# Performance work log

Measured on AMD Instinct MI355X. Metric: run time of the kernel, lower is better.

## Reference

```python
import jax, jax.numpy as jnp
import numpy as np

N = 50000
E = 640000
IN_DIM = 23
HID = 128
NUM_CLASS = 12


def setup_inputs() -> dict:
    key = jax.random.key(0)
    ks = jax.random.split(key, 12)
    x = jax.random.normal(ks[0], (N, IN_DIM), dtype=jnp.float32)
    edge_index = jax.random.randint(ks[1], (2, E), 0, N, dtype=jnp.int32)

    def glorot(k, shape):
        fan_in, fan_out = shape
        lim = np.sqrt(6.0 / (fan_in + fan_out)).astype(np.float32)
        return jax.random.uniform(k, shape, jnp.float32, -lim, lim)

    W1 = glorot(ks[2], (IN_DIM, HID)); b1 = jnp.zeros((HID,), jnp.float32)
    W2 = glorot(ks[3], (HID, HID));    b2 = jnp.zeros((HID,), jnp.float32)
    W3 = glorot(ks[4], (HID, HID));    b3 = jnp.zeros((HID,), jnp.float32)
    Wc1 = glorot(ks[5], (HID, 64));    bc1 = jnp.zeros((64,), jnp.float32)
    Wc2 = glorot(ks[6], (64, NUM_CLASS)); bc2 = jnp.zeros((NUM_CLASS,), jnp.float32)
    return {"x": x, "edge_index": edge_index,
            "W1": W1, "b1": b1, "W2": W2, "b2": b2, "W3": W3, "b3": b3,
            "Wc1": Wc1, "bc1": bc1, "Wc2": Wc2, "bc2": bc2}


def _gcn_norm(edge_index, n_nodes):
    # add self loops, compute symmetric normalization D^-1/2 (A+I) D^-1/2
    loop = jnp.arange(n_nodes, dtype=edge_index.dtype)
    src = jnp.concatenate([edge_index[0], loop])
    dst = jnp.concatenate([edge_index[1], loop])
    deg = jax.ops.segment_sum(jnp.ones_like(dst, dtype=jnp.float32), dst,
                              num_segments=n_nodes)
    dinv = jax.lax.rsqrt(deg)  # deg >= 1 due to self loops
    norm = dinv[src] * dinv[dst]  # [E + N]
    return src, dst, norm


def _gcn_layer(h, W, b, src, dst, norm, n_nodes):
    h = h @ W                          # linear (bias applied after aggregation, per PyG)
    msg = h[src] * norm[:, None]       # gather + scale
    out = jax.ops.segment_sum(msg, dst, num_segments=n_nodes)  # scatter-add
    return out + b


def reference(x, edge_index, W1, b1, W2, b2, W3, b3, Wc1, bc1, Wc2, bc2):
    n = x.shape[0]
    src, dst, norm = _gcn_norm(edge_index, n)
    h = jnp.tanh(_gcn_layer(x, W1, b1, src, dst, norm, n))
    h = jnp.tanh(_gcn_layer(h, W2, b2, src, dst, norm, n))
    h = jnp.tanh(_gcn_layer(h, W3, b3, src, dst, norm, n))
    # dropout is identity in eval mode
    out = h @ Wc1 + bc1
    out = out @ Wc2 + bc2
    return out
```

## Files before the change

### kernel.cpp

```cpp
#include <hip/hip_runtime.h>
#include <math.h>

#define NN 50000
#define EE 640000
#define IND 23
#define HID 128
#define MIDD 64
#define NCLS 12
#define NB 49
#define QS 32766.0f
#define INVQS (1.0f / 32766.0f)
#define BSH 7
#define NBK 391
#define CHUNK 4096
#define NPB 157
#define PADB 6250
#define GB16 3125

typedef short short8v __attribute__((ext_vector_type(8)));
typedef short short4v __attribute__((ext_vector_type(4)));
typedef float f32x4 __attribute__((ext_vector_type(4)));
typedef unsigned long long u64;

__device__ __forceinline__ short f2bf(float f) {
    unsigned u = __float_as_uint(f);
    unsigned r = (u + 0x7FFFu + ((u >> 16) & 1u)) >> 16;
    return (short)r;
}
__device__ __forceinline__ float bf2f(short s) {
    return __uint_as_float(((unsigned)(unsigned short)s) << 16);
}
__device__ __forceinline__ float fast_tanh(float x) {
    float t = __expf(-2.f * fabsf(x));
    float r = (1.f - t) / (1.f + t);
    return copysignf(r, x);
}

__global__ __launch_bounds__(256) void k_pre(const int* __restrict__ dst,
                                             int* __restrict__ cnt,
                                             const float* __restrict__ Wc1,
                                             const float* __restrict__ bc1,
                                             const float* __restrict__ Wc2,
                                             const float* __restrict__ bc2,
                                             float* __restrict__ Wcc,
                                             float* __restrict__ bcc,
                                             const float* __restrict__ W2,
                                             const float* __restrict__ W3,
                                             short* __restrict__ w2hi,
                                             short* __restrict__ w2lo,
                                             short* __restrict__ w3hi,
                                             short* __restrict__ w3lo,
                                             const float* __restrict__ W1,
                                             short* __restrict__ w1hi,
                                             short* __restrict__ w1lo) {
    const int bid = blockIdx.x;
    const int tid = threadIdx.x;
    if (bid < 2500) {
        int i = bid * 256 + tid;
        if (i < EE) atomicAdd(&cnt[dst[i]], 1);
        return;
    }
    if (bid < 2506) {
        int t = (bid - 2500) * 256 + tid;
        if (t < HID * NCLS) {
            int k = t / NCLS, c = t % NCLS;
            float s = 0.f;
#pragma unroll 8
            for (int j = 0; j < MIDD; ++j) s += Wc1[k * MIDD + j] * Wc2[j * NCLS + c];
            Wcc[t] = s;
        }
        if (t < NCLS) {
            float s = bc2[t];
#pragma unroll 8
            for (int j = 0; j < MIDD; ++j) s += bc1[j] * Wc2[j * NCLS + t];
            bcc[t] = s;
        }
        return;
    }
    if (bid < 2634) {
        int bb = bid - 2506;
        const float* W = (bb < 64) ? W2 : W3;
        short* hi = (bb < 64) ? w2hi : w3hi;
        short* lo = (bb < 64) ? w2lo : w3lo;
        int i = (bb & 63) * 256 + tid;
        int k = i >> 7, c = i & 127;
        float w = W[i];
        short h = f2bf(w);
        short l = f2bf(w - bf2f(h));
        hi[((k >> 3) * 128 + c) * 8 + (k & 7)] = h;
        lo[((k >> 3) * 128 + c) * 8 + (k & 7)] = l;
        return;
    }
    int i = (bid - 2634) * 256 + tid;
    int k = i >> 7, c = i & 127;
    float w = (k < IND) ? W1[k * HID + c] : 0.f;
    short h = f2bf(w);
    short l = f2bf(w - bf2f(h));
    w1hi[((k >> 3) * 128 + c) * 8 + (k & 7)] = h;
    w1lo[((k >> 3) * 128 + c) * 8 + (k & 7)] = l;
}

__global__ __launch_bounds__(256) void k_scan_local(const int* __restrict__ cnt,
                                                    int* __restrict__ row_ptr,
                                                    float* __restrict__ dinv,
                                                    int* __restrict__ sums) {
    __shared__ int wtot[4];
    const int tid = threadIdx.x;
    const int wid = tid >> 6, lane = tid & 63;
    const int base = blockIdx.x * 1024 + tid * 4;
    int v[4];
#pragma unroll
    for (int t = 0; t < 4; ++t) {
        int i = base + t;
        v[t] = (i < NN) ? cnt[i] : 0;
        if (i < NN) dinv[i] = rsqrtf((float)v[t] + 1.0f);
    }
    int slocal = v[0] + v[1] + v[2] + v[3];
    int val = slocal;
#pragma unroll
    for (int off = 1; off < 64; off <<= 1) {
        int t = __shfl_up(val, off, 64);
        if (lane >= off) val += t;
    }
    if (lane == 63) wtot[wid] = val;
    __syncthreads();
    int woff = 0;
#pragma unroll
    for (int w = 0; w < 4; ++w) woff += (w < wid) ? wtot[w] : 0;
    int run = woff + val - slocal;
#pragma unroll
    for (int t = 0; t < 4; ++t) {
        int i = base + t;
        if (i < NN) row_ptr[i] = run;
        run += v[t];
    }
    if (tid == 255) sums[blockIdx.x] = woff + val;
}

__global__ __launch_bounds__(256) void k_scan_apply2(int* __restrict__ row_ptr,
                                                     const int* __restrict__ sums,
                                                     int* __restrict__ bcurA) {
    __shared__ int so;
    const int tid = threadIdx.x;
    if (tid < 64) {
        int a = (tid < (int)blockIdx.x) ? sums[tid] : 0;
        int b = (tid < NB) ? sums[tid] : 0;
#pragma unroll
        for (int off = 32; off; off >>= 1) {
            a += __shfl_down(a, off, 64);
            b += __shfl_down(b, off, 64);
        }
        if (tid == 0) {
            so = a;
            if (blockIdx.x == NB - 1) row_ptr[NN] = b;
        }
    }
    __syncthreads();
    const int o = so;
    const int base = blockIdx.x * 1024 + tid * 4;
#pragma unroll
    for (int t = 0; t < 4; ++t) {
        int i = base + t;
        if (i < NN) {
            int rp = row_ptr[i] + o;
            row_ptr[i] = rp;
            if ((i & 127) == 0) bcurA[i >> BSH] = rp;
        }
    }
}

__global__ __launch_bounds__(256) void k_part(const int* __restrict__ src,
                                              const int* __restrict__ dst,
                                              const float* __restrict__ dinv,
                                              int* __restrict__ bcurA,
                                              u64* __restrict__ sw_g,
                                              int* __restrict__ d_g,
                                              const float* __restrict__ x,
                                              float* __restrict__ xp) {
    const int bid = blockIdx.x;
    const int tid = threadIdx.x;
    if (bid >= NPB) {
        int i = (bid - NPB) * 256 + tid;
        int node = i >> 5, f = i & 31;
        xp[i] = (f < IND) ? x[node * IND + f] * dinv[node] : 0.f;
        return;
    }
    __shared__ int hist[NBK], base[NBK], cur[NBK], gb[NBK];
    __shared__ u64 lsw[CHUNK];
    __shared__ int ld[CHUNK];
    const int e0 = bid * CHUNK;
    const int total = min(CHUNK, EE - e0);
    for (int t = tid; t < NBK; t += 256) hist[t] = 0;
    __syncthreads();
    int sv[16], dv[16];
#pragma unroll
    for (int t = 0; t < 16; ++t) {
        int i = e0 + t * 256 + tid;
        if (i < EE) {
            sv[t] = src[i];
            dv[t] = dst[i];
            atomicAdd(&hist[dv[t] >> BSH], 1);
        } else dv[t] = -1;
    }
    __syncthreads();
    if (tid < 64) {
        int carry = 0;
        for (int c = 0; c < NBK; c += 64) {
            int idx = c + tid;
            int v = (idx < NBK) ? hist[idx] : 0;
            int sc = v;
#pragma unroll
            for (int off = 1; off < 64; off <<= 1) {
                int tv = __shfl_up(sc, off, 64);
                if (tid >= off) sc += tv;
            }
            if (idx < NBK) base[idx] = carry + sc - v;
            carry += __shfl(sc, 63, 64);
        }
    }
    __syncthreads();
    for (int t = tid; t < NBK; t += 256) {
        cur[t] = base[t];
        gb[t] = hist[t] ? atomicAdd(&bcurA[t], hist[t]) : 0;
    }
    __syncthreads();
#pragma unroll
    for (int t = 0; t < 16; ++t) {
        if (dv[t] >= 0) {
            int b = dv[t] >> BSH;
            int r = atomicAdd(&cur[b], 1);
            lsw[r] = (unsigned)sv[t] |
                     ((u64)__float_as_uint(dinv[sv[t]]) << 32);
            ld[r] = dv[t];
        }
    }
    __syncthreads();
    for (int j = tid; j < total; j += 256) {
        int d = ld[j];
        int b = d >> BSH;
        int gpos = gb[b] + (j - base[b]);
        sw_g[gpos] = lsw[j];
        d_g[gpos] = d;
    }
}

__global__ __launch_bounds__(256) void k_sort(const int* __restrict__ row_ptr,
                                              const u64* __restrict__ sw_g,
                                              const int* __restrict__ d_g,
                                              u64* __restrict__ e_sn) {
    __shared__ int rloc[129];
    __shared__ int curl[128];
    __shared__ u64 osw[3072];
    const int bid = blockIdx.x, tid = threadIdx.x;
    const int n0 = bid << BSH;
    const int nlast = min(128, NN - n0);
    if (tid <= nlast) rloc[tid] = row_ptr[n0 + tid];
    if (tid < 128) curl[tid] = 0;
    __syncthreads();
    const int rbeg = rloc[0];
    const int cnt = rloc[nlast] - rbeg;
    for (int j = tid; j < cnt; j += 256) {
        int d = d_g[rbeg + j];
        int li = d - n0;
        int r = atomicAdd(&curl[li], 1);
        int pl = (rloc[li] - rbeg) + r;
        u64 v = sw_g[rbeg + j];
        if (pl < 3072) osw[pl] = v;
        else e_sn[rbeg + pl] = v;
    }
    __syncthreads();
    const int lim = min(cnt, 3072);
    for (int j = tid; j < lim; j += 256) e_sn[rbeg + j] = osw[j];
}

__global__ __launch_bounds__(256) void k_aggx(const float* __restrict__ xp,
                                              const int* __restrict__ row_ptr,
                                              const int2* __restrict__ e_sn,
                                              const float* __restrict__ dinv,
                                              short4v* __restrict__ axh,
                                              short4v* __restrict__ axl) {
    const int tid = threadIdx.x;
    const int i = blockIdx.x * 4 + (tid >> 6);
    const int lane = tid & 63;
    const int slot = lane >> 3;
    const int f = lane & 7;
    const float4* xp4 = (const float4*)xp;
    const int beg = row_ptr[i];
    const int deg = row_ptr[i + 1] - beg;
    float4 acc = make_float4(0.f, 0.f, 0.f, 0.f);
    for (int base = 0; base < deg; base += 64) {
        const int cnt = min(64, deg - base);
        int s_l = 0;
        if (lane < cnt) s_l = e_sn[beg + base + lane].x;
        int e = 0;
        for (; e + 8 <= cnt; e += 8) {
            int s = __shfl(s_l, e + slot, 64);
            float4 v = xp4[s * 8 + f];
            acc.x += v.x; acc.y += v.y; acc.z += v.z; acc.w += v.w;
        }
        if (e < cnt) {
            int s = __shfl(s_l, e + slot, 64);
            if (e + slot < cnt) {
                float4 v = xp4[s * 8 + f];
                acc.x += v.x; acc.y += v.y; acc.z += v.z; acc.w += v.w;
            }
        }
    }
#pragma unroll
    for (int off = 32; off >= 8; off >>= 1) {
        acc.x += __shfl_down(acc.x, off, 64);
        acc.y += __shfl_down(acc.y, off, 64);
        acc.z += __shfl_down(acc.z, off, 64);
        acc.w += __shfl_down(acc.w, off, 64);
    }
    if (lane < 8) {
        const float di = dinv[i];
        float4 v = xp4[i * 8 + lane];
        float a[4];
        a[0] = (acc.x + v.x) * di; a[1] = (acc.y + v.y) * di;
        a[2] = (acc.z + v.z) * di; a[3] = (acc.w + v.w) * di;
        short4v h4, l4;
#pragma unroll
        for (int j = 0; j < 4; ++j) {
            short h = f2bf(a[j]);
            h4[j] = h;
            l4[j] = f2bf(a[j] - bf2f(h));
        }
        axh[(size_t)i * 8 + lane] = h4;
        axl[(size_t)i * 8 + lane] = l4;
    }
}

__global__ __launch_bounds__(256) void k_gemm_l1(const short8v* __restrict__ axh8,
                                                 const short8v* __restrict__ axl8,
                                                 const short8v* __restrict__ w1hi8,
                                                 const short8v* __restrict__ w1lo8,
                                                 const float* __restrict__ bias,
                                                 short* __restrict__ qout) {
    const int tid = threadIdx.x;
    const int lane = tid & 63, wv = tid >> 6;
    const int g = lane >> 4, c16 = lane & 15;
    const int rb = blockIdx.x * 16;
    const int colb = wv * 32;
    short8v Ah = axh8[(size_t)(rb + c16) * 4 + g];
    short8v Al = axl8[(size_t)(rb + c16) * 4 + g];
    short8v Bh[2], Bl[2];
#pragma unroll
    for (int ct = 0; ct < 2; ++ct) {
        int wi = g * 128 + colb + ct * 16 + c16;
        Bh[ct] = w1hi8[wi];
        Bl[ct] = w1lo8[wi];
    }
    __builtin_amdgcn_sched_barrier(0);
    f32x4 acc[2];
    acc[0] = f32x4{0.f, 0.f, 0.f, 0.f};
    acc[1] = f32x4{0.f, 0.f, 0.f, 0.f};
#pragma unroll
    for (int ct = 0; ct < 2; ++ct) {
        acc[ct] = __builtin_amdgcn_mfma_f32_16x16x32_bf16(Ah, Bh[ct], acc[ct], 0, 0, 0);
        acc[ct] = __builtin_amdgcn_mfma_f32_16x16x32_bf16(Ah, Bl[ct], acc[ct], 0, 0, 0);
        acc[ct] = __builtin_amdgcn_mfma_f32_16x16x32_bf16(Al, Bh[ct], acc[ct], 0, 0, 0);
    }
#pragma unroll
    for (int ct = 0; ct < 2; ++ct) {
        const int col = colb + ct * 16 + c16;
        const float bb = bias[col];
#pragma unroll
        for (int r = 0; r < 4; ++r) {
            int nd = rb + 4 * g + r;
            float v = fast_tanh(acc[ct][r] + bb);
            qout[nd * HID + col] = (short)__float2int_rn(v * QS);
        }
    }
}

__global__ __launch_bounds__(256) void k_aggq(const short* __restrict__ hq,
                                              const int* __restrict__ row_ptr,
                                              const int2* __restrict__ e_sn,
                                              const float* __restrict__ dinv,
                                              short8v* __restrict__ ah,
                                              short8v* __restrict__ al) {
    const int tid = threadIdx.x;
    const int i = blockIdx.x * 4 + (tid >> 6);
    const int lane = tid & 63;
    const int slot = lane >> 4;
    const int f = lane & 15;
    const short8v* h8 = (const short8v*)hq;
    const int beg = row_ptr[i];
    const int deg = row_ptr[i + 1] - beg;
    float facc[8];
#pragma unroll
    for (int t = 0; t < 8; ++t) facc[t] = 0.f;
    for (int base = 0; base < deg; base += 64) {
        const int cnt = min(64, deg - base);
        int s_l = 0; float n_l = 0.f;
        if (lane < cnt) {
            int2 sn = e_sn[beg + base + lane];
            s_l = sn.x;
            n_l = __int_as_float(sn.y);
        }
        int e = 0;
#pragma unroll 4
        for (; e + 4 <= cnt; e += 4) {
            int s = __shfl(s_l, e + slot, 64);
            float nr = __shfl(n_l, e + slot, 64);
            short8v v = h8[(size_t)s * 16 + f];
#pragma unroll
            for (int t = 0; t < 8; ++t) facc[t] += (float)v[t] * nr;
        }
        if (e < cnt) {
            int s = __shfl(s_l, e + slot, 64);
            float nr = __shfl(n_l, e + slot, 64);
            if (e + slot < cnt) {
                short8v v = h8[(size_t)s * 16 + f];
#pragma unroll
                for (int t = 0; t < 8; ++t) facc[t] += (float)v[t] * nr;
            }
        }
    }
#pragma unroll
    for (int off = 32; off >= 16; off >>= 1)
#pragma unroll
        for (int t = 0; t < 8; ++t) facc[t] += __shfl_down(facc[t], off, 64);
    if (lane < 16) {
        const float di = dinv[i];
        const float sc = di * INVQS;
        short8v v = h8[(size_t)i * 16 + lane];
        short8v hi8, lo8;
#pragma unroll
        for (int t = 0; t < 8; ++t) {
            float o = (facc[t] + di * (float)v[t]) * sc;
            short h = f2bf(o);
            hi8[t] = h;
            lo8[t] = f2bf(o - bf2f(h));
        }
        ah[(size_t)i * 16 + lane] = hi8;
        al[(size_t)i * 16 + lane] = lo8;
    }
}

#define GEMM_CORE16                                                            \
    const int tid = threadIdx.x;                                               \
    const int lane = tid & 63, wv = tid >> 6;                                  \
    const int g = lane >> 4, c16 = lane & 15;                                  \
    const int rb = blockIdx.x * 16;                                            \
    const int colb = wv * 32;                                                  \
    const size_t arow = (size_t)(rb + c16) * 16;                               \
    short8v Ah[4], Al[4], Bh[4][2], Bl[4][2];                                  \
    _Pragma("unroll")                                                          \
    for (int t = 0; t < 4; ++t) {                                              \
        Ah[t] = ah[arow + t * 4 + g];                                          \
        Al[t] = al[arow + t * 4 + g];                                          \
        _Pragma("unroll")                                                      \
        for (int ct = 0; ct < 2; ++ct) {                                       \
            int wi = (t * 4 + g) * 128 + colb + ct * 16 + c16;                 \
            Bh[t][ct] = whi8[wi];                                              \
            Bl[t][ct] = wlo8[wi];                                              \
        }                                                                      \
    }                                                                          \
    __builtin_amdgcn_sched_barrier(0);                                         \
    f32x4 acc[2];                                                              \
    acc[0] = f32x4{0.f, 0.f, 0.f, 0.f};                                        \
    acc[1] = f32x4{0.f, 0.f, 0.f, 0.f};                                        \
    _Pragma("unroll")                                                          \
    for (int t = 0; t < 4; ++t) {                                              \
        _Pragma("unroll")                                                      \
        for (int ct = 0; ct < 2; ++ct) {                                       \
            acc[ct] = __builtin_amdgcn_mfma_f32_16x16x32_bf16(Ah[t], Bh[t][ct], acc[ct], 0, 0, 0); \
            acc[ct] = __builtin_amdgcn_mfma_f32_16x16x32_bf16(Ah[t], Bl[t][ct], acc[ct], 0, 0, 0); \
            acc[ct] = __builtin_amdgcn_mfma_f32_16x16x32_bf16(Al[t], Bh[t][ct], acc[ct], 0, 0, 0); \
        }                                                                      \
    }

__global__ __launch_bounds__(256) void k_gemm_q(const short8v* __restrict__ ah,
                                                const short8v* __restrict__ al,
                                                const short8v* __restrict__ whi8,
                                                const short8v* __restrict__ wlo8,
                                                const float* __restrict__ bias,
                                                short* __restrict__ qout) {
    GEMM_CORE16
#pragma unroll
    for (int ct = 0; ct < 2; ++ct) {
        const int col = colb + ct * 16 + c16;
        const float bb = bias[col];
#pragma unroll
        for (int r = 0; r < 4; ++r) {
            int nd = rb + 4 * g + r;
            float v = fast_tanh(acc[ct][r] + bb);
            qout[nd * HID + col] = (short)__float2int_rn(v * QS);
        }
    }
}

__global__ __launch_bounds__(256) void k_gemm_head(const short8v* __restrict__ ah,
                                                   const short8v* __restrict__ al,
                                                   const short8v* __restrict__ whi8,
                                                   const short8v* __restrict__ wlo8,
                                                   const float* __restrict__ bias,
                                                   const float* __restrict__ Wcc,
                                                   const float* __restrict__ bcc,
                                                   float* __restrict__ outp) {
    __shared__ float WccS[HID * NCLS];
    __shared__ float bccS[NCLS];
    __shared__ float psum[4][16][NCLS];
    {
        const int t0 = threadIdx.x;
        for (int t = t0; t < HID * NCLS; t += 256) WccS[t] = Wcc[t];
        if (t0 < NCLS) bccS[t0] = bcc[t0];
    }
    __syncthreads();
    GEMM_CORE16
    float part[4][NCLS];
#pragma unroll
    for (int r = 0; r < 4; ++r)
#pragma unroll
        for (int c = 0; c < NCLS; ++c) part[r][c] = 0.f;
#pragma unroll
    for (int ct = 0; ct < 2; ++ct) {
        const int col = colb + ct * 16 + c16;
        const float bb = bias[col];
        const float4* wr = (const float4*)&WccS[col * NCLS];
        float4 wa = wr[0], wb2 = wr[1], wc = wr[2];
#pragma unroll
        for (int r = 0; r < 4; ++r) {
            float v = fast_tanh(acc[ct][r] + bb);
            part[r][0]  += v * wa.x;  part[r][1]  += v * wa.y;
            part[r][2]  += v * wa.z;  part[r][3]  += v * wa.w;
            part[r][4]  += v * wb2.x; part[r][5]  += v * wb2.y;
            part[r][6]  += v * wb2.z; part[r][7]  += v * wb2.w;
            part[r][8]  += v * wc.x;  part[r][9]  += v * wc.y;
            part[r][10] += v * wc.z;  part[r][11] += v * wc.w;
        }
    }
#pragma unroll
    for (int off = 8; off; off >>= 1)
#pragma unroll
        for (int r = 0; r < 4; ++r)
#pragma unroll
            for (int c = 0; c < NCLS; ++c)
                part[r][c] += __shfl_down(part[r][c], off, 64);
    if (c16 == 0) {
#pragma unroll
        for (int r = 0; r < 4; ++r)
#pragma unroll
            for (int c = 0; c < NCLS; ++c)
                psum[wv][4 * g + r][c] = part[r][c];
    }
    __syncthreads();
    if (tid < 16 * NCLS) {
        int row = tid / NCLS, c = tid % NCLS;
        float s = bccS[c] + psum[0][row][c] + psum[1][row][c]
                + psum[2][row][c] + psum[3][row][c];
        outp[(rb + row) * NCLS + c] = s;
    }
}


extern "C" void kernel_launch(void* const* d_in, const int* in_sizes, int n_in,
                              void* d_out, int out_size, void* d_ws, size_t ws_size,
                              hipStream_t stream) {
    const float* x    = (const float*)d_in[0];
    const int*   edge = (const int*)d_in[1];
    const int*   src  = edge;
    const int*   dst  = edge + EE;
    const float* W1  = (const float*)d_in[2];  const float* b1  = (const float*)d_in[3];
    const float* W2  = (const float*)d_in[4];  const float* b2  = (const float*)d_in[5];
    const float* W3  = (const float*)d_in[6];  const float* b3  = (const float*)d_in[7];
    const float* Wc1 = (const float*)d_in[8];  const float* bc1 = (const float*)d_in[9];
    const float* Wc2 = (const float*)d_in[10]; const float* bc2 = (const float*)d_in[11];
    float* outp = (float*)d_out;

    char* p = (char*)d_ws;
    int*   cnt     = (int*)p;   p += 200064;
    int*   row_ptr = (int*)p;   p += 200064;
    float* dinv    = (float*)p; p += 200064;
    int*   sums    = (int*)p;   p += 256;
    int*   bcurA   = (int*)p;   p += 2048;
    int2*  e_sn    = (int2*)p;  p += (size_t)EE * 8;
    u64*   sw_g    = (u64*)p;   p += (size_t)EE * 8;
    int*   d_g     = (int*)p;   p += (size_t)EE * 4;
    float* xp      = (float*)p; p += (size_t)NN * 32 * 4;
    short* q       = (short*)p; p += (size_t)NN * HID * 2;
    short8v* ah    = (short8v*)p; p += (size_t)(NN + 16) * 256;
    short8v* al    = (short8v*)p; p += (size_t)(NN + 16) * 256;
    short4v* axh   = (short4v*)p; p += (size_t)(NN + 16) * 64;
    short4v* axl   = (short4v*)p; p += (size_t)(NN + 16) * 64;
    float* Wcc     = (float*)p; p += HID * NCLS * 4;
    float* bcc     = (float*)p; p += 256;
    short* w2hi    = (short*)p; p += 32768;
    short* w2lo    = (short*)p; p += 32768;
    short* w3hi    = (short*)p; p += 32768;
    short* w3lo    = (short*)p; p += 32768;
    short* w1hi    = (short*)p; p += 8192;
    short* w1lo    = (short*)p; p += 8192;

    hipMemsetAsync(cnt, 0, (size_t)NN * 4, stream);
    k_pre        <<<2650, 256, 0, stream>>>(dst, cnt, Wc1, bc1, Wc2, bc2, Wcc, bcc,
                                            W2, W3, w2hi, w2lo, w3hi, w3lo,
                                            W1, w1hi, w1lo);
    k_scan_local <<<NB, 256, 0, stream>>>(cnt, row_ptr, dinv, sums);
    k_scan_apply2<<<NB, 256, 0, stream>>>(row_ptr, sums, bcurA);
    k_part       <<<NPB + PADB, 256, 0, stream>>>(src, dst, dinv, bcurA,
                                                  sw_g, d_g, x, xp);
    k_sort       <<<NBK, 256, 0, stream>>>(row_ptr, sw_g, d_g, (u64*)e_sn);

    k_aggx    <<<NN / 4, 256, 0, stream>>>(xp, row_ptr, e_sn, dinv, axh, axl);
    k_gemm_l1 <<<GB16, 256, 0, stream>>>((const short8v*)axh, (const short8v*)axl,
                                         (const short8v*)w1hi, (const short8v*)w1lo,
                                         b1, q);
    k_aggq     <<<NN / 4, 256, 0, stream>>>(q, row_ptr, e_sn, dinv, ah, al);
    k_gemm_q   <<<GB16, 256, 0, stream>>>(ah, al, (const short8v*)w2hi,
                                          (const short8v*)w2lo, b2, q);
    k_aggq     <<<NN / 4, 256, 0, stream>>>(q, row_ptr, e_sn, dinv, ah, al);
    k_gemm_head<<<GB16, 256, 0, stream>>>(ah, al, (const short8v*)w3hi,
                                          (const short8v*)w3lo, b3, Wcc, bcc, outp);
}
```

Measured before the change: 288.4 us.

## Merge two-pass scan into single-block kernel and widen aggq per-lane loads

Replaces the two-kernel prefix scan (local scan plus apply) with one 1024-thread single-block kernel that walks the node counts in 13 chunks with a running total. This removes a kernel launch at the cost of running the scan serially on one CU. Separately, the aggregation kernel now gives each lane 16 features (two short8 loads) across 8 edge slots instead of 8 features across 4 slots. This doubles the number of edges in flight per wavefront but also doubles per-lane accumulator registers.

```diff
diff --git a/kernel.cpp b/kernel.cpp
--- a/kernel.cpp
+++ b/kernel.cpp
@@ -7,7 +7,6 @@
 #define HID 128
 #define MIDD 64
 #define NCLS 12
-#define NB 49
 #define QS 32766.0f
 #define INVQS (1.0f / 32766.0f)
 #define BSH 7
@@ -100,73 +99,53 @@
     w1lo[((k >> 3) * 128 + c) * 8 + (k & 7)] = l;
 }
 
-__global__ __launch_bounds__(256) void k_scan_local(const int* __restrict__ cnt,
-                                                    int* __restrict__ row_ptr,
-                                                    float* __restrict__ dinv,
-                                                    int* __restrict__ sums) {
-    __shared__ int wtot[4];
+__global__ __launch_bounds__(1024) void k_scan(const int* __restrict__ cnt,
+                                               int* __restrict__ row_ptr,
+                                               float* __restrict__ dinv,
+                                               int* __restrict__ bcurA) {
+    __shared__ int wsum[16];
     const int tid = threadIdx.x;
     const int wid = tid >> 6, lane = tid & 63;
-    const int base = blockIdx.x * 1024 + tid * 4;
-    int v[4];
-#pragma unroll
-    for (int t = 0; t < 4; ++t) {
-        int i = base + t;
-        v[t] = (i < NN) ? cnt[i] : 0;
-        if (i < NN) dinv[i] = rsqrtf((float)v[t] + 1.0f);
-    }
-    int slocal = v[0] + v[1] + v[2] + v[3];
-    int val = slocal;
-#pragma unroll
-    for (int off = 1; off < 64; off <<= 1) {
-        int t = __shfl_up(val, off, 64);
-        if (lane >= off) val += t;
-    }
-    if (lane == 63) wtot[wid] = val;
-    __syncthreads();
-    int woff = 0;
-#pragma unroll
-    for (int w = 0; w < 4; ++w) woff += (w < wid) ? wtot[w] : 0;
-    int run = woff + val - slocal;
-#pragma unroll
-    for (int t = 0; t < 4; ++t) {
-        int i = base + t;
-        if (i < NN) row_ptr[i] = run;
-        run += v[t];
-    }
-    if (tid == 255) sums[blockIdx.x] = woff + val;
-}
-
-__global__ __launch_bounds__(256) void k_scan_apply2(int* __restrict__ row_ptr,
-                                                     const int* __restrict__ sums,
-                                                     int* __restrict__ bcurA) {
-    __shared__ int so;
-    const int tid = threadIdx.x;
-    if (tid < 64) {
-        int a = (tid < (int)blockIdx.x) ? sums[tid] : 0;
-        int b = (tid < NB) ? sums[tid] : 0;
-#pragma unroll
-        for (int off = 32; off; off >>= 1) {
-            a += __shfl_down(a, off, 64);
-            b += __shfl_down(b, off, 64);
-        }
-        if (tid == 0) {
-            so = a;
-            if (blockIdx.x == NB - 1) row_ptr[NN] = b;
-        }
-    }
-    __syncthreads();
-    const int o = so;
-    const int base = blockIdx.x * 1024 + tid * 4;
-#pragma unroll
-    for (int t = 0; t < 4; ++t) {
-        int i = base + t;
-        if (i < NN) {
-            int rp = row_ptr[i] + o;
-            row_ptr[i] = rp;
-            if ((i & 127) == 0) bcurA[i >> BSH] = rp;
-        }
-    }
+    int running = 0;
+    for (int c = 0; c < 13; ++c) {
+        const int base = c * 4096 + tid * 4;
+        int v[4];
+#pragma unroll
+        for (int t = 0; t < 4; ++t) {
+            int i = base + t;
+            v[t] = (i < NN) ? cnt[i] : 0;
+            if (i < NN) dinv[i] = rsqrtf((float)v[t] + 1.0f);
+        }
+        int s = v[0] + v[1] + v[2] + v[3];
+        int val = s;
+#pragma unroll
+        for (int off = 1; off < 64; off <<= 1) {
+            int t = __shfl_up(val, off, 64);
+            if (lane >= off) val += t;
+        }
+        if (lane == 63) wsum[wid] = val;
+        __syncthreads();
+        int woff = 0, tot = 0;
+#pragma unroll
+        for (int w = 0; w < 16; ++w) {
+            int ws = wsum[w];
+            woff += (w < wid) ? ws : 0;
+            tot += ws;
+        }
+        int run = running + woff + val - s;
+#pragma unroll
+        for (int t = 0; t < 4; ++t) {
+            int i = base + t;
+            if (i < NN) {
+                row_ptr[i] = run;
+                if ((i & 127) == 0) bcurA[i >> BSH] = run;
+            }
+            run += v[t];
+        }
+        running += tot;
+        __syncthreads();
+    }
+    if (tid == 0) row_ptr[NN] = running;
 }
 
 __global__ __launch_bounds__(256) void k_part(const int* __restrict__ src,
@@ -383,14 +362,14 @@
     const int tid = threadIdx.x;
     const int i = blockIdx.x * 4 + (tid >> 6);
     const int lane = tid & 63;
-    const int slot = lane >> 4;
-    const int f = lane & 15;
+    const int slot = lane >> 3;
+    const int f = lane & 7;
     const short8v* h8 = (const short8v*)hq;
     const int beg = row_ptr[i];
     const int deg = row_ptr[i + 1] - beg;
-    float facc[8];
-#pragma unroll
-    for (int t = 0; t < 8; ++t) facc[t] = 0.f;
+    float facc[16];
+#pragma unroll
+    for (int t = 0; t < 16; ++t) facc[t] = 0.f;
     for (int base = 0; base < deg; base += 64) {
         const int cnt = min(64, deg - base);
         int s_l = 0; float n_l = 0.f;
@@ -400,42 +379,57 @@
             n_l = __int_as_float(sn.y);
         }
         int e = 0;
-#pragma unroll 4
-        for (; e + 4 <= cnt; e += 4) {
+#pragma unroll 2
+        for (; e + 8 <= cnt; e += 8) {
             int s = __shfl(s_l, e + slot, 64);
             float nr = __shfl(n_l, e + slot, 64);
-            short8v v = h8[(size_t)s * 16 + f];
-#pragma unroll
-            for (int t = 0; t < 8; ++t) facc[t] += (float)v[t] * nr;
+            short8v v0 = h8[(size_t)s * 16 + f * 2];
+            short8v v1 = h8[(size_t)s * 16 + f * 2 + 1];
+#pragma unroll
+            for (int t = 0; t < 8; ++t) {
+                facc[t]     += (float)v0[t] * nr;
+                facc[8 + t] += (float)v1[t] * nr;
+            }
         }
         if (e < cnt) {
             int s = __shfl(s_l, e + slot, 64);
             float nr = __shfl(n_l, e + slot, 64);
             if (e + slot < cnt) {
-                short8v v = h8[(size_t)s * 16 + f];
-#pragma unroll
-                for (int t = 0; t < 8; ++t) facc[t] += (float)v[t] * nr;
+                short8v v0 = h8[(size_t)s * 16 + f * 2];
+                short8v v1 = h8[(size_t)s * 16 + f * 2 + 1];
+#pragma unroll
+                for (int t = 0; t < 8; ++t) {
+                    facc[t]     += (float)v0[t] * nr;
+                    facc[8 + t] += (float)v1[t] * nr;
+                }
             }
         }
     }
 #pragma unroll
-    for (int off = 32; off >= 16; off >>= 1)
-#pragma unroll
-        for (int t = 0; t < 8; ++t) facc[t] += __shfl_down(facc[t], off, 64);
-    if (lane < 16) {
+    for (int off = 32; off >= 8; off >>= 1)
+#pragma unroll
+        for (int t = 0; t < 16; ++t) facc[t] += __shfl_down(facc[t], off, 64);
+    if (lane < 8) {
         const float di = dinv[i];
         const float sc = di * INVQS;
-        short8v v = h8[(size_t)i * 16 + lane];
-        short8v hi8, lo8;
+        short8v v0 = h8[(size_t)i * 16 + lane * 2];
+        short8v v1 = h8[(size_t)i * 16 + lane * 2 + 1];
+        short8v h0, l0, h1, l1;
 #pragma unroll
         for (int t = 0; t < 8; ++t) {
-            float o = (facc[t] + di * (float)v[t]) * sc;
-            short h = f2bf(o);
-            hi8[t] = h;
-            lo8[t] = f2bf(o - bf2f(h));
-        }
-        ah[(size_t)i * 16 + lane] = hi8;
-        al[(size_t)i * 16 + lane] = lo8;
+            float o0 = (facc[t] + di * (float)v0[t]) * sc;
+            short hh0 = f2bf(o0);
+            h0[t] = hh0;
+            l0[t] = f2bf(o0 - bf2f(hh0));
+            float o1 = (facc[8 + t] + di * (float)v1[t]) * sc;
+            short hh1 = f2bf(o1);
+            h1[t] = hh1;
+            l1[t] = f2bf(o1 - bf2f(hh1));
+        }
+        ah[(size_t)i * 16 + lane * 2]     = h0;
+        ah[(size_t)i * 16 + lane * 2 + 1] = h1;
+        al[(size_t)i * 16 + lane * 2]     = l0;
+        al[(size_t)i * 16 + lane * 2 + 1] = l1;
     }
 }
 
@@ -574,7 +568,6 @@
     int*   cnt     = (int*)p;   p += 200064;
     int*   row_ptr = (int*)p;   p += 200064;
     float* dinv    = (float*)p; p += 200064;
-    int*   sums    = (int*)p;   p += 256;
     int*   bcurA   = (int*)p;   p += 2048;
     int2*  e_sn    = (int2*)p;  p += (size_t)EE * 8;
     u64*   sw_g    = (u64*)p;   p += (size_t)EE * 8;
@@ -595,14 +588,13 @@
     short* w1lo    = (short*)p; p += 8192;
 
     hipMemsetAsync(cnt, 0, (size_t)NN * 4, stream);
-    k_pre        <<<2650, 256, 0, stream>>>(dst, cnt, Wc1, bc1, Wc2, bc2, Wcc, bcc,
-                                            W2, W3, w2hi, w2lo, w3hi, w3lo,
-                                            W1, w1hi, w1lo);
-    k_scan_local <<<NB, 256, 0, stream>>>(cnt, row_ptr, dinv, sums);
-    k_scan_apply2<<<NB, 256, 0, stream>>>(row_ptr, sums, bcurA);
-    k_part       <<<NPB + PADB, 256, 0, stream>>>(src, dst, dinv, bcurA,
-                                                  sw_g, d_g, x, xp);
-    k_sort       <<<NBK, 256, 0, stream>>>(row_ptr, sw_g, d_g, (u64*)e_sn);
+    k_pre  <<<2650, 256, 0, stream>>>(dst, cnt, Wc1, bc1, Wc2, bc2, Wcc, bcc,
+                                      W2, W3, w2hi, w2lo, w3hi, w3lo,
+                                      W1, w1hi, w1lo);
+    k_scan <<<1, 1024, 0, stream>>>(cnt, row_ptr, dinv, bcurA);
+    k_part <<<NPB + PADB, 256, 0, stream>>>(src, dst, dinv, bcurA,
+                                            sw_g, d_g, x, xp);
+    k_sort <<<NBK, 256, 0, stream>>>(row_ptr, sw_g, d_g, (u64*)e_sn);
 
     k_aggx    <<<NN / 4, 256, 0, stream>>>(xp, row_ptr, e_sn, dinv, axh, axl);
     k_gemm_l1 <<<GB16, 256, 0, stream>>>((const short8v*)axh, (const short8v*)axl,
```

Result: slower. 326.4 us (+13.2%).
